# Kernel tuning notes

Hardware: AMD Instinct MI355X
Metric: run time of the kernel (lower is better)

## Reference

```python
import jax, jax.numpy as jnp
import numpy as np

B, H, Wd, C = 8, 64, 64, 128
KH, KW = 3, 3
N = KH * KW  # kernel_n
F = 256


def _grid_offset(h, w, kh, kw):
    """Replicates the TensorLayer grid construction exactly, including the
    (2,kh,kw)->(kh*kw,2) reshape of the stacked meshgrid."""
    n = kh * kw
    initial = np.stack(np.meshgrid(np.arange(kh), np.arange(kw), indexing='ij'))  # (2,kh,kw)
    initial = initial.reshape(-1, 2).astype(np.float32)  # (n,2), faithful flattening order
    gy = np.arange(-int((kh - 1) / 2.0), h - int((kh - 1) / 2.0))
    gx = np.arange(-int((kw - 1) / 2.0), w - int((kw - 1) / 2.0))
    grid = np.stack(np.meshgrid(gy, gx, indexing='ij'), axis=-1).astype(np.float32)  # (h,w,2)
    grid = np.tile(grid[:, :, None, :], (1, 1, n, 1))  # (h,w,n,2)
    return jnp.asarray(grid + initial[None, None, :, :])  # (h,w,n,2)


def setup_inputs() -> dict:
    key = jax.random.key(0)
    k1, k2, k3 = jax.random.split(key, 3)
    x = jax.random.normal(k1, (B, H, Wd, C), dtype=jnp.float32)
    offsets = jax.random.normal(k2, (B, H, Wd, 2 * N), dtype=jnp.float32)
    W = jax.random.normal(k3, (N, C, F), dtype=jnp.float32) * 0.02  # truncated_normal(0.02) analogue
    b = jnp.zeros((F,), dtype=jnp.float32)
    return {"x": x, "offsets": offsets, "W": W, "b": b}


def reference(x, offsets, W, b):
    h, w = x.shape[1], x.shape[2]
    grid = _grid_offset(h, w, KH, KW)  # (h,w,n,2)
    coords = grid[None] + offsets.reshape(x.shape[0], h, w, N, 2)  # (b,h,w,n,2)
    cy = jnp.clip(coords[..., 0], 0.0, jnp.float32(h - 1))
    cx = jnp.clip(coords[..., 1], 0.0, jnp.float32(w - 1))
    y0 = jnp.floor(cy).astype(jnp.int32)
    y1 = jnp.ceil(cy).astype(jnp.int32)
    x0 = jnp.floor(cx).astype(jnp.int32)
    x1 = jnp.ceil(cx).astype(jnp.int32)

    bidx = jnp.arange(x.shape[0])[:, None, None, None]

    def gather(yy, xx):
        return x[bidx, yy, xx]  # (b,h,w,n,c)

    v_lt = gather(y0, x0)
    v_rb = gather(y1, x1)
    v_lb = gather(y0, x1)  # (lt_y, rb_x) as in original
    v_rt = gather(y1, x0)  # (rb_y, lt_x) as in original

    fy = (cy - y0.astype(cy.dtype))[..., None]
    fx = (cx - x0.astype(cx.dtype))[..., None]
    vals_t = v_lt + (v_rt - v_lt) * fy
    vals_b = v_lb + (v_rb - v_lb) * fy
    mapped = vals_t + (vals_b - vals_t) * fx  # (b,h,w,n,c)

    # conv3d with kernel [1,1,n,c,f] + VALID == contraction over (n,c)
    out = jnp.einsum('bhwnc,ncf->bhwf', mapped, W) + b
    return out
```

## Files before the change

### kernel.cpp

```cpp
#include <hip/hip_runtime.h>

#define HH 64
#define WW 64
#define CC 128
#define FF 256
#define NTAP 9
#define KD 1152
#define XELEMS (8 * HH * WW * CC)
#define XCVT_BLOCKS (XELEMS / (256 * 8))
#define WT_BLOCKS 144

typedef __attribute__((ext_vector_type(8))) short bf16x8;
typedef __attribute__((ext_vector_type(4))) float floatx4;

__device__ inline unsigned short f2bf(float v) {
  union { float f; unsigned u; } c; c.f = v;
  unsigned r = (c.u + 0x7FFFu + ((c.u >> 16) & 1u)) >> 16;
  return (unsigned short)r;
}
__device__ inline float bflo(unsigned u) {
  union { unsigned u; float f; } c; c.u = u << 16; return c.f;
}
__device__ inline float bfhi(unsigned u) {
  union { unsigned u; float f; } c; c.u = u & 0xFFFF0000u; return c.f;
}
__device__ inline unsigned cvt_pk_bf16(float lo, float hi) {
  unsigned r;
  asm("v_cvt_pk_bf16_f32 %0, %1, %2" : "=v"(r) : "v"(lo), "v"(hi));
  return r;
}

__device__ inline unsigned lerp_word(unsigned u00, unsigned u10, unsigned u01, unsigned u11,
                                     float fy, float fx) {
  float v00 = bflo(u00), v10 = bflo(u10), v01 = bflo(u01), v11 = bflo(u11);
  float tx = v00 + (v10 - v00) * fy;
  float tb = v01 + (v11 - v01) * fy;
  float rlo = tx + (tb - tx) * fx;
  v00 = bfhi(u00); v10 = bfhi(u10); v01 = bfhi(u01); v11 = bfhi(u11);
  tx = v00 + (v10 - v00) * fy;
  tb = v01 + (v11 - v01) * fy;
  float rhi = tx + (tb - tx) * fx;
  return cvt_pk_bf16(rlo, rhi);
}

#define IY_PACK 0x18690
#define IX_PACK 0x21894

struct ITap { int b00, b10, b01, b11; float fy, fx; };

__device__ inline ITap interp_setup(const float* __restrict__ offp, int i, int p, int nx) {
  const int n = nx >> 1;
  const float2 o2 = *(const float2*)(offp + 2 * n);
  float cy = (float)(i - 1 + ((IY_PACK >> (2 * n)) & 3)) + o2.x;
  float cx = (float)(p - 1 + ((IX_PACK >> (2 * n)) & 3)) + o2.y;
  cy = fminf(fmaxf(cy, 0.f), 63.f);
  cx = fminf(fmaxf(cx, 0.f), 63.f);
  const float fy0 = floorf(cy), fx0 = floorf(cx);
  const int y0 = (int)fy0, y1 = (int)ceilf(cy);
  const int x0 = (int)fx0, x1 = (int)ceilf(cx);
  ITap t;
  t.b00 = (y0 * WW + x0) * CC;
  t.b10 = (y1 * WW + x0) * CC;
  t.b01 = (y0 * WW + x1) * CC;
  t.b11 = (y1 * WW + x1) * CC;
  t.fy = cy - fy0;
  t.fx = cx - fx0;
  return t;
}

__global__ void prep_kernel(const float* __restrict__ X, const float* __restrict__ W,
                            unsigned short* __restrict__ Xb, unsigned short* __restrict__ Wt) {
  const int blk = blockIdx.x;
  if (blk < XCVT_BLOCKS) {
    const int t = blk * 256 + threadIdx.x;
    const float4* src = (const float4*)(X + (size_t)t * 8);
    float4 a = src[0], b2 = src[1];
    bf16x8 o;
    o[0] = (short)f2bf(a.x);  o[1] = (short)f2bf(a.y);
    o[2] = (short)f2bf(a.z);  o[3] = (short)f2bf(a.w);
    o[4] = (short)f2bf(b2.x); o[5] = (short)f2bf(b2.y);
    o[6] = (short)f2bf(b2.z); o[7] = (short)f2bf(b2.w);
    *(bf16x8*)(Xb + (size_t)t * 8) = o;
  } else {
    const int t = (blk - XCVT_BLOCKS) * 256 + threadIdx.x;
    const int f = t & 255;
    const int k0 = (t >> 8) * 8;
    unsigned short o[8];
#pragma unroll
    for (int i2 = 0; i2 < 8; ++i2)
      o[i2] = f2bf(W[(size_t)(k0 + i2) * FF + f]);
    *(uint4*)(Wt + (size_t)f * KD + k0) = *(uint4*)o;
  }
}

__global__ __launch_bounds__(512, 4) void fused_kernel(
    const unsigned short* __restrict__ Xb, const float* __restrict__ Off,
    const unsigned short* __restrict__ Wt, const float* __restrict__ bias,
    float* __restrict__ Out)
{
  __shared__ unsigned short smA[64 * 64];
  __shared__ unsigned short smB[256 * 64];

  const int blk = blockIdx.x;
  const int b   = blk & 7;
  const int i   = blk >> 3;
  const int m0  = (b * 64 + i) * 64;
  const int tid = threadIdx.x;
  const int wave = tid >> 6, lane = tid & 63;
  const int wm   = (wave & 1) * 32;
  const int wf   = (wave >> 1) * 64;
  const int arow = lane & 15, aq = lane >> 4;
  const int p  = tid >> 3;
  const int c0 = tid & 7;

  const unsigned short* xb = Xb + (size_t)b * (HH * WW * CC);
  const float* offp = Off + ((size_t)(b * 64 + i) * 64 + p) * (2 * NTAP);

  floatx4 acc[2][4];
#pragma unroll
  for (int mt = 0; mt < 2; ++mt)
#pragma unroll
    for (int ft = 0; ft < 4; ++ft)
      acc[mt][ft] = (floatx4){0.f, 0.f, 0.f, 0.f};

#define STAGE_B(KT)                                                                  \
  {                                                                                  \
    _Pragma("unroll")                                                                \
    for (int q2 = 0; q2 < 4; ++q2) {                                                 \
      const int row = q2 * 64 + (tid >> 3);                                          \
      const int chp = c0 ^ (row & 7);                                                \
      const unsigned short* gp = Wt + (size_t)row * KD + (KT) * 64 + chp * 8;        \
      unsigned short* l = (unsigned short*)&smB[row * 64 + c0 * 8];                  \
      __builtin_amdgcn_global_load_lds(                                              \
          (const __attribute__((address_space(1))) unsigned int*)gp,                 \
          (__attribute__((address_space(3))) unsigned int*)l, 16, 0, 0);             \
    }                                                                                \
  }

  {
    ITap t = interp_setup(offp, i, p, 0);
    const int ch = c0 * 8;
    uint4 q00 = *(const uint4*)(xb + t.b00 + ch);
    uint4 q10 = *(const uint4*)(xb + t.b10 + ch);
    uint4 q01 = *(const uint4*)(xb + t.b01 + ch);
    uint4 q11 = *(const uint4*)(xb + t.b11 + ch);
    unsigned ow0 = lerp_word(q00.x, q10.x, q01.x, q11.x, t.fy, t.fx);
    unsigned ow1 = lerp_word(q00.y, q10.y, q01.y, q11.y, t.fy, t.fx);
    unsigned ow2 = lerp_word(q00.z, q10.z, q01.z, q11.z, t.fy, t.fx);
    unsigned ow3 = lerp_word(q00.w, q10.w, q01.w, q11.w, t.fy, t.fx);
    *(uint4*)&smA[p * 64 + ((c0 ^ (p & 7)) << 3)] = make_uint4(ow0, ow1, ow2, ow3);
    STAGE_B(0)
  }
  __syncthreads();

  for (int kt = 0; kt < 18; ++kt) {
    bf16x8 afr[2][2], bfr[2][4];
#pragma unroll
    for (int ks = 0; ks < 2; ++ks) {
      const int slot = (((ks * 4 + aq) ^ (arow & 7)) << 3);
#pragma unroll
      for (int mt = 0; mt < 2; ++mt)
        afr[ks][mt] = *(const bf16x8*)&smA[(wm + mt * 16 + arow) * 64 + slot];
#pragma unroll
      for (int ft = 0; ft < 4; ++ft)
        bfr[ks][ft] = *(const bf16x8*)&smB[(wf + ft * 16 + arow) * 64 + slot];
    }
    __syncthreads();

    const int nx = kt + 1;
    ITap t;
    uint4 g00, g10, g01, g11;
    if (nx < 18) {
      t = interp_setup(offp, i, p, nx);
      const int ch = ((nx & 1) * 8 + c0) * 8;
      g00 = *(const uint4*)(xb + t.b00 + ch);
      g10 = *(const uint4*)(xb + t.b10 + ch);
      g01 = *(const uint4*)(xb + t.b01 + ch);
      g11 = *(const uint4*)(xb + t.b11 + ch);
      STAGE_B(nx)
    }

#pragma unroll
    for (int ks = 0; ks < 2; ++ks)
#pragma unroll
      for (int mt = 0; mt < 2; ++mt)
#pragma unroll
        for (int ft = 0; ft < 4; ++ft)
          acc[mt][ft] = __builtin_amdgcn_mfma_f32_16x16x32_bf16(
              afr[ks][mt], bfr[ks][ft], acc[mt][ft], 0, 0, 0);

    if (nx < 18) {
      unsigned ow0 = lerp_word(g00.x, g10.x, g01.x, g11.x, t.fy, t.fx);
      unsigned ow1 = lerp_word(g00.y, g10.y, g01.y, g11.y, t.fy, t.fx);
      unsigned ow2 = lerp_word(g00.z, g10.z, g01.z, g11.z, t.fy, t.fx);
      unsigned ow3 = lerp_word(g00.w, g10.w, g01.w, g11.w, t.fy, t.fx);
      *(uint4*)&smA[p * 64 + ((c0 ^ (p & 7)) << 3)] = make_uint4(ow0, ow1, ow2, ow3);
    }
    __syncthreads();
  }
#undef STAGE_B

  float bv[4];
#pragma unroll
  for (int ft = 0; ft < 4; ++ft)
    bv[ft] = bias[wf + ft * 16 + arow];
#pragma unroll
  for (int mt = 0; mt < 2; ++mt) {
#pragma unroll
    for (int ft = 0; ft < 4; ++ft) {
      const int f = wf + ft * 16 + arow;
#pragma unroll
      for (int r = 0; r < 4; ++r) {
        const int m = m0 + wm + mt * 16 + aq * 4 + r;
        Out[(size_t)m * FF + f] = acc[mt][ft][r] + bv[ft];
      }
    }
  }
}

extern "C" void kernel_launch(void* const* d_in, const int* in_sizes, int n_in,
                              void* d_out, int out_size, void* d_ws, size_t ws_size,
                              hipStream_t stream) {
  const float* X    = (const float*)d_in[0];
  const float* Off  = (const float*)d_in[1];
  const float* W    = (const float*)d_in[2];
  const float* bias = (const float*)d_in[3];
  float* Out = (float*)d_out;

  unsigned short* Wt = (unsigned short*)d_ws;
  unsigned short* Xb = Wt + (size_t)FF * KD;

  prep_kernel<<<XCVT_BLOCKS + WT_BLOCKS, 256, 0, stream>>>(X, W, Xb, Wt);
  fused_kernel<<<512, 512, 0, stream>>>(Xb, Off, Wt, bias, Out);
}
```

Measured before the change: 112.6 us.

## Double-buffer LDS tiles, reuse tap setup across K halves, use 4-weight bilinear

```diff
diff --git a/kernel.cpp b/kernel.cpp
--- a/kernel.cpp
+++ b/kernel.cpp
@@ -30,27 +30,12 @@
   return r;
 }
 
-__device__ inline unsigned lerp_word(unsigned u00, unsigned u10, unsigned u01, unsigned u11,
-                                     float fy, float fx) {
-  float v00 = bflo(u00), v10 = bflo(u10), v01 = bflo(u01), v11 = bflo(u11);
-  float tx = v00 + (v10 - v00) * fy;
-  float tb = v01 + (v11 - v01) * fy;
-  float rlo = tx + (tb - tx) * fx;
-  v00 = bfhi(u00); v10 = bfhi(u10); v01 = bfhi(u01); v11 = bfhi(u11);
-  tx = v00 + (v10 - v00) * fy;
-  tb = v01 + (v11 - v01) * fy;
-  float rhi = tx + (tb - tx) * fx;
-  return cvt_pk_bf16(rlo, rhi);
-}
-
 #define IY_PACK 0x18690
 #define IX_PACK 0x21894
 
-struct ITap { int b00, b10, b01, b11; float fy, fx; };
-
-__device__ inline ITap interp_setup(const float* __restrict__ offp, int i, int p, int nx) {
-  const int n = nx >> 1;
-  const float2 o2 = *(const float2*)(offp + 2 * n);
+struct ITap { int b00, b10, b01, b11; float w00, w10, w01, w11; };
+
+__device__ inline ITap tap_from(float2 o2, int i, int p, int n) {
   float cy = (float)(i - 1 + ((IY_PACK >> (2 * n)) & 3)) + o2.x;
   float cx = (float)(p - 1 + ((IX_PACK >> (2 * n)) & 3)) + o2.y;
   cy = fminf(fmaxf(cy, 0.f), 63.f);
@@ -58,14 +43,25 @@
   const float fy0 = floorf(cy), fx0 = floorf(cx);
   const int y0 = (int)fy0, y1 = (int)ceilf(cy);
   const int x0 = (int)fx0, x1 = (int)ceilf(cx);
+  const float fy = cy - fy0, fx = cx - fx0;
+  const float gy0 = 1.f - fy, gx0 = 1.f - fx;
   ITap t;
   t.b00 = (y0 * WW + x0) * CC;
   t.b10 = (y1 * WW + x0) * CC;
   t.b01 = (y0 * WW + x1) * CC;
   t.b11 = (y1 * WW + x1) * CC;
-  t.fy = cy - fy0;
-  t.fx = cx - fx0;
+  t.w00 = gy0 * gx0;
+  t.w10 = fy  * gx0;
+  t.w01 = gy0 * fx;
+  t.w11 = fy  * fx;
   return t;
+}
+
+__device__ inline unsigned lerp_word(unsigned u00, unsigned u10, unsigned u01, unsigned u11,
+                                     const ITap& t) {
+  float rlo = bflo(u00) * t.w00 + bflo(u10) * t.w10 + bflo(u01) * t.w01 + bflo(u11) * t.w11;
+  float rhi = bfhi(u00) * t.w00 + bfhi(u10) * t.w10 + bfhi(u01) * t.w01 + bfhi(u11) * t.w11;
+  return cvt_pk_bf16(rlo, rhi);
 }
 
 __global__ void prep_kernel(const float* __restrict__ X, const float* __restrict__ W,
@@ -98,8 +94,8 @@
     const unsigned short* __restrict__ Wt, const float* __restrict__ bias,
     float* __restrict__ Out)
 {
-  __shared__ unsigned short smA[64 * 64];
-  __shared__ unsigned short smB[256 * 64];
+  __shared__ unsigned short smA[2][64 * 64];
+  __shared__ unsigned short smB[2][256 * 64];
 
   const int blk = blockIdx.x;
   const int b   = blk & 7;
@@ -114,7 +110,7 @@
   const int c0 = tid & 7;
 
   const unsigned short* xb = Xb + (size_t)b * (HH * WW * CC);
-  const float* offp = Off + ((size_t)(b * 64 + i) * 64 + p) * (2 * NTAP);
+  const float* offp = Off + ((size_t)(b * HH + i) * WW + p) * (2 * NTAP);
 
   floatx4 acc[2][4];
 #pragma unroll
@@ -123,36 +119,37 @@
     for (int ft = 0; ft < 4; ++ft)
       acc[mt][ft] = (floatx4){0.f, 0.f, 0.f, 0.f};
 
-#define STAGE_B(KT)                                                                  \
+#define STAGE_B(KT, BUF)                                                             \
   {                                                                                  \
     _Pragma("unroll")                                                                \
-    for (int q2 = 0; q2 < 4; ++q2) {                                                 \
-      const int row = q2 * 64 + (tid >> 3);                                          \
+    for (int pass = 0; pass < 4; ++pass) {                                           \
+      const int row = pass * 64 + (tid >> 3);                                        \
       const int chp = c0 ^ (row & 7);                                                \
       const unsigned short* gp = Wt + (size_t)row * KD + (KT) * 64 + chp * 8;        \
-      unsigned short* l = (unsigned short*)&smB[row * 64 + c0 * 8];                  \
+      unsigned short* l = (unsigned short*)&smB[BUF][row * 64 + c0 * 8];             \
       __builtin_amdgcn_global_load_lds(                                              \
           (const __attribute__((address_space(1))) unsigned int*)gp,                 \
           (__attribute__((address_space(3))) unsigned int*)l, 16, 0, 0);             \
     }                                                                                \
   }
 
+  ITap t = tap_from(*(const float2*)offp, i, p, 0);
+  STAGE_B(0, 0)
   {
-    ITap t = interp_setup(offp, i, p, 0);
     const int ch = c0 * 8;
     uint4 q00 = *(const uint4*)(xb + t.b00 + ch);
     uint4 q10 = *(const uint4*)(xb + t.b10 + ch);
     uint4 q01 = *(const uint4*)(xb + t.b01 + ch);
     uint4 q11 = *(const uint4*)(xb + t.b11 + ch);
-    unsigned ow0 = lerp_word(q00.x, q10.x, q01.x, q11.x, t.fy, t.fx);
-    unsigned ow1 = lerp_word(q00.y, q10.y, q01.y, q11.y, t.fy, t.fx);
-    unsigned ow2 = lerp_word(q00.z, q10.z, q01.z, q11.z, t.fy, t.fx);
-    unsigned ow3 = lerp_word(q00.w, q10.w, q01.w, q11.w, t.fy, t.fx);
-    *(uint4*)&smA[p * 64 + ((c0 ^ (p & 7)) << 3)] = make_uint4(ow0, ow1, ow2, ow3);
-    STAGE_B(0)
+    unsigned w0 = lerp_word(q00.x, q10.x, q01.x, q11.x, t);
+    unsigned w1 = lerp_word(q00.y, q10.y, q01.y, q11.y, t);
+    unsigned w2 = lerp_word(q00.z, q10.z, q01.z, q11.z, t);
+    unsigned w3 = lerp_word(q00.w, q10.w, q01.w, q11.w, t);
+    *(uint4*)&smA[0][p * 64 + ((c0 ^ (p & 7)) << 3)] = make_uint4(w0, w1, w2, w3);
   }
   __syncthreads();
 
+  int cur = 0;
   for (int kt = 0; kt < 18; ++kt) {
     bf16x8 afr[2][2], bfr[2][4];
 #pragma unroll
@@ -160,24 +157,23 @@
       const int slot = (((ks * 4 + aq) ^ (arow & 7)) << 3);
 #pragma unroll
       for (int mt = 0; mt < 2; ++mt)
-        afr[ks][mt] = *(const bf16x8*)&smA[(wm + mt * 16 + arow) * 64 + slot];
+        afr[ks][mt] = *(const bf16x8*)&smA[cur][(wm + mt * 16 + arow) * 64 + slot];
 #pragma unroll
       for (int ft = 0; ft < 4; ++ft)
-        bfr[ks][ft] = *(const bf16x8*)&smB[(wf + ft * 16 + arow) * 64 + slot];
-    }
-    __syncthreads();
-
-    const int nx = kt + 1;
-    ITap t;
-    uint4 g00, g10, g01, g11;
-    if (nx < 18) {
-      t = interp_setup(offp, i, p, nx);
-      const int ch = ((nx & 1) * 8 + c0) * 8;
-      g00 = *(const uint4*)(xb + t.b00 + ch);
-      g10 = *(const uint4*)(xb + t.b10 + ch);
-      g01 = *(const uint4*)(xb + t.b01 + ch);
-      g11 = *(const uint4*)(xb + t.b11 + ch);
-      STAGE_B(nx)
+        bfr[ks][ft] = *(const bf16x8*)&smB[cur][(wf + ft * 16 + arow) * 64 + slot];
+    }
+
+    const int nk = kt + 1;
+    uint4 g0, g1, g2, g3;
+    if (nk < 18) {
+      if ((nk & 1) == 0)
+        t = tap_from(*(const float2*)(offp + 2 * (nk >> 1)), i, p, nk >> 1);
+      const int ch = ((nk & 1) * 8 + c0) * 8;
+      g0 = *(const uint4*)(xb + t.b00 + ch);
+      g1 = *(const uint4*)(xb + t.b10 + ch);
+      g2 = *(const uint4*)(xb + t.b01 + ch);
+      g3 = *(const uint4*)(xb + t.b11 + ch);
+      STAGE_B(nk, cur ^ 1)
     }
 
 #pragma unroll
@@ -189,14 +185,15 @@
           acc[mt][ft] = __builtin_amdgcn_mfma_f32_16x16x32_bf16(
               afr[ks][mt], bfr[ks][ft], acc[mt][ft], 0, 0, 0);
 
-    if (nx < 18) {
-      unsigned ow0 = lerp_word(g00.x, g10.x, g01.x, g11.x, t.fy, t.fx);
-      unsigned ow1 = lerp_word(g00.y, g10.y, g01.y, g11.y, t.fy, t.fx);
-      unsigned ow2 = lerp_word(g00.z, g10.z, g01.z, g11.z, t.fy, t.fx);
-      unsigned ow3 = lerp_word(g00.w, g10.w, g01.w, g11.w, t.fy, t.fx);
-      *(uint4*)&smA[p * 64 + ((c0 ^ (p & 7)) << 3)] = make_uint4(ow0, ow1, ow2, ow3);
+    if (nk < 18) {
+      unsigned w0 = lerp_word(g0.x, g1.x, g2.x, g3.x, t);
+      unsigned w1 = lerp_word(g0.y, g1.y, g2.y, g3.y, t);
+      unsigned w2 = lerp_word(g0.z, g1.z, g2.z, g3.z, t);
+      unsigned w3 = lerp_word(g0.w, g1.w, g2.w, g3.w, t);
+      *(uint4*)&smA[cur ^ 1][p * 64 + ((c0 ^ (p & 7)) << 3)] = make_uint4(w0, w1, w2, w3);
     }
     __syncthreads();
+    cur ^= 1;
   }
 #undef STAGE_B
 
```

Result: no change. 112.4 us (-0.2%).
